# Kernel optimization log

Measured on AMD Instinct MI355X. Metric: run time of the kernel, lower is better.

## Reference

```python
import jax, jax.numpy as jnp
import numpy as np

EPS = 1e-6
ALPHA = 0.2  # LeakyReLU negative slope


def layer_norm(x, g, b):
    mu = jnp.mean(x, axis=-1, keepdims=True)
    var = jnp.mean(jnp.square(x - mu), axis=-1, keepdims=True)
    return (x - mu) * jax.lax.rsqrt(var + EPS) * g + b


def graph_attention(x, bias, W, a_src, a_dst):
    # x: [B,N,D], bias: [B,N,N], W: [D, H*Dh], a_src/a_dst: [H, Dh]
    B, N, D = x.shape
    H, Dh = a_src.shape
    h = jnp.einsum('bnd,dhk->bhnk', x, W.reshape(D, H, Dh))  # [B,H,N,Dh]
    s = jnp.einsum('bhnk,hk->bhn', h, a_src)                 # source term
    t = jnp.einsum('bhnk,hk->bhn', h, a_dst)                 # target term
    e = jax.nn.leaky_relu(s[:, :, :, None] + t[:, :, None, :], ALPHA)
    e = e + bias[:, None, :, :]                              # graph mask/bias
    attn = jax.nn.softmax(e, axis=-1)                        # [B,H,N,N]
    out = jnp.einsum('bhij,bhjk->bhik', attn, h)             # [B,H,N,Dh]
    return out.transpose(0, 2, 1, 3).reshape(B, N, H * Dh)


def setup_inputs() -> dict:
    key = jax.random.key(0)
    ks = jax.random.split(key, 8)
    B, N, D, H = 2, 2048, 512, 8
    Dh = D // H
    sc = 1.0 / np.sqrt(D)
    return {
        'x': jax.random.normal(ks[0], (B, N, D), jnp.float32),
        'bias': jax.random.normal(ks[1], (B, N, N), jnp.float32),
        'W1': jax.random.normal(ks[2], (D, D), jnp.float32) * sc,
        'a_src1': jax.random.normal(ks[3], (H, Dh), jnp.float32) * sc,
        'a_dst1': jax.random.normal(ks[4], (H, Dh), jnp.float32) * sc,
        'g1': jnp.ones((D,), jnp.float32),
        'b1': jnp.zeros((D,), jnp.float32),
        'W2': jax.random.normal(ks[5], (D, D), jnp.float32) * sc,
        'a_src2': jax.random.normal(ks[6], (1, D), jnp.float32) * sc,
        'a_dst2': jax.random.normal(ks[7], (1, D), jnp.float32) * sc,
        'g2': jnp.ones((D,), jnp.float32),
        'b2': jnp.zeros((D,), jnp.float32),
    }


def reference(x, bias, W1, a_src1, a_dst1, g1, b1, W2, a_src2, a_dst2, g2, b2):
    # dropout is identity in eval mode
    attn_in = layer_norm(x, g1, b1)
    attn = graph_attention(attn_in, bias, W1, a_src1, a_dst1) + x
    attn_in2 = layer_norm(attn, g2, b2)
    out = graph_attention(attn_in2, bias, W2, a_src2, a_dst2) + attn
    return out
```

## Files before the change

kernel.cpp:

```cpp
#include <hip/hip_runtime.h>
#include <math.h>

#define NB 2
#define NN 2048
#define DD 512

typedef __attribute__((ext_vector_type(8))) short short8;
typedef __attribute__((ext_vector_type(4))) float f32x4;

__device__ __forceinline__ unsigned short f2bf(float x) {
  union { float f; unsigned u; } a;
  a.f = x;
  unsigned r = a.u + 0x7FFF + ((a.u >> 16) & 1);
  return (unsigned short)(r >> 16);
}
__device__ __forceinline__ float bf2f(unsigned short u) {
  union { unsigned u; float f; } a;
  a.u = ((unsigned)u) << 16;
  return a.f;
}
__device__ __forceinline__ unsigned cvtpk(float lo, float hi) {
  unsigned r;
  asm("v_cvt_pk_bf16_f32 %0, %1, %2" : "=v"(r) : "v"(lo), "v"(hi));
  return r;
}

__device__ __forceinline__ float waveReduceSum(float v) {
#pragma unroll
  for (int o = 32; o; o >>= 1) v += __shfl_down(v, o, 64);
  return v;
}
__device__ __forceinline__ float waveReduceMax(float v) {
#pragma unroll
  for (int o = 32; o; o >>= 1) v = fmaxf(v, __shfl_down(v, o, 64));
  return v;
}
__device__ __forceinline__ float blockReduceSum(float v, float* red4) {
  int tid = threadIdx.x;
  __syncthreads();
  v = waveReduceSum(v);
  if ((tid & 63) == 0) red4[tid >> 6] = v;
  __syncthreads();
  return red4[0] + red4[1] + red4[2] + red4[3];
}
__device__ __forceinline__ float blockReduceMax(float v, float* red4) {
  int tid = threadIdx.x;
  __syncthreads();
  v = waveReduceMax(v);
  if ((tid & 63) == 0) red4[tid >> 6] = v;
  __syncthreads();
  return fmaxf(fmaxf(red4[0], red4[1]), fmaxf(red4[2], red4[3]));
}

__global__ __launch_bounds__(256) void ln_kernel(const float* __restrict__ x,
                                                 const float* __restrict__ g,
                                                 const float* __restrict__ bb,
                                                 unsigned short* __restrict__ y) {
  int row = blockIdx.x;
  int t = threadIdx.x;
  const float* xr = x + (size_t)row * DD;
  __shared__ float red4[4];
  float2 v = *(const float2*)&xr[2 * t];
  float s = blockReduceSum(v.x + v.y, red4);
  float mu = s * (1.0f / 512.0f);
  float d0 = v.x - mu, d1 = v.y - mu;
  float ss = blockReduceSum(d0 * d0 + d1 * d1, red4);
  float rstd = rsqrtf(ss * (1.0f / 512.0f) + 1e-6f);
  float2 gg = *(const float2*)&g[2 * t];
  float2 bv = *(const float2*)&bb[2 * t];
  ushort2 o;
  o.x = f2bf(d0 * rstd * gg.x + bv.x);
  o.y = f2bf(d1 * rstd * gg.y + bv.y);
  *(ushort2*)&y[(size_t)row * DD + 2 * t] = o;
}

__global__ __launch_bounds__(256) void wt2_kernel(const float* __restrict__ W1,
                                                  const float* __restrict__ W2,
                                                  unsigned short* __restrict__ WT1,
                                                  unsigned short* __restrict__ WT2) {
  const float* W = blockIdx.z ? W2 : W1;
  unsigned short* WT = blockIdx.z ? WT2 : WT1;
  __shared__ float tile[64][65];
  int kt = blockIdx.x * 64, ct = blockIdx.y * 64;
  int t = threadIdx.x;
#pragma unroll
  for (int u = 0; u < 16; u++) {
    int lin = t + u * 256;
    int kl = lin >> 6, cl = lin & 63;
    tile[kl][cl] = W[(size_t)(kt + kl) * DD + ct + cl];
  }
  __syncthreads();
#pragma unroll
  for (int u = 0; u < 16; u++) {
    int lin = t + u * 256;
    int cl = lin >> 6, kl = lin & 63;
    WT[(size_t)(ct + cl) * DD + kt + kl] = f2bf(tile[kl][cl]);
  }
}

__global__ __launch_bounds__(256) void v2_kernel(
    const float* __restrict__ W1, const float* __restrict__ as1,
    const float* __restrict__ ad1, float* __restrict__ vs1, float* __restrict__ vd1,
    const float* __restrict__ W2, const float* __restrict__ as2,
    const float* __restrict__ ad2, float* __restrict__ vs2, float* __restrict__ vd2) {
  int slot = blockIdx.y;
  const float *W, *as, *ad;
  float *vs, *vd;
  int Dh, hoff;
  if (slot < 8) {
    W = W1; as = as1 + slot * 64; ad = ad1 + slot * 64;
    vs = vs1 + (size_t)slot * DD; vd = vd1 + (size_t)slot * DD;
    Dh = 64; hoff = slot * 64;
  } else {
    W = W2; as = as2; ad = ad2; vs = vs2; vd = vd2;
    Dh = 512; hoff = 0;
  }
  int t = threadIdx.x;
  int dl = t >> 2, kq = t & 3;
  int d = blockIdx.x * 64 + dl;
  int kn = Dh >> 2;
  const float* wr = W + (size_t)d * DD + hoff + kq * kn;
  const float* asp = as + kq * kn;
  const float* adp = ad + kq * kn;
  float s = 0.f, dd2 = 0.f;
  for (int k = 0; k < kn; k++) {
    float wv = wr[k];
    s += wv * asp[k];
    dd2 += wv * adp[k];
  }
  s += __shfl_xor(s, 1);
  s += __shfl_xor(s, 2);
  dd2 += __shfl_xor(dd2, 1);
  dd2 += __shfl_xor(dd2, 2);
  if (kq == 0) {
    vs[d] = s;
    vd[d] = dd2;
  }
}

__global__ __launch_bounds__(256) void bmax_kernel(const float* __restrict__ bias,
                                                   float* __restrict__ bmax) {
  int row = blockIdx.x;
  int t = threadIdx.x;
  __shared__ float red4[4];
  const float* br = bias + (size_t)row * NN;
  float4 a = *(const float4*)&br[t * 4];
  float4 c = *(const float4*)&br[t * 4 + 1024];
  float lm = fmaxf(fmaxf(fmaxf(a.x, a.y), fmaxf(a.z, a.w)),
                   fmaxf(fmaxf(c.x, c.y), fmaxf(c.z, c.w)));
  float m = blockReduceMax(lm, red4);
  if (t == 0) bmax[row] = m;
}

__global__ __launch_bounds__(256) void gemm_kernel(const unsigned short* __restrict__ A,
                                                   const unsigned short* __restrict__ BT,
                                                   unsigned short* __restrict__ hbT) {
  __shared__ float accL[4][16][65];
  int t = threadIdx.x, w = t >> 6, l = t & 63;
  int li = l & 15, lg = l >> 4;
  int R0 = blockIdx.x * 16;
  int c0 = blockIdx.y * 64;
  const unsigned short* ar = A + (size_t)(R0 + li) * DD + w * 128 + lg * 8;
  const unsigned short* br = BT + (size_t)(c0 + li) * DD + w * 128 + lg * 8;
  f32x4 acc[4] = {};
#pragma unroll
  for (int k0 = 0; k0 < 128; k0 += 32) {
    short8 af = *(const short8*)(ar + k0);
#pragma unroll
    for (int f = 0; f < 4; f++) {
      short8 bf = *(const short8*)(br + (size_t)f * 16 * DD + k0);
      acc[f] = __builtin_amdgcn_mfma_f32_16x16x32_bf16(af, bf, acc[f], 0, 0, 0);
    }
  }
#pragma unroll
  for (int f = 0; f < 4; f++)
#pragma unroll
    for (int r = 0; r < 4; r++) accL[w][lg * 4 + r][f * 16 + li] = acc[f][r];
  __syncthreads();
  int b = R0 >> 11, jT = (R0 & (NN - 1)) >> 4;
  int cT0 = c0 >> 4;
#pragma unroll
  for (int u = 0; u < 2; u++) {
    int idx = t + u * 256;
    int f = idx >> 7;
    int rem = idx & 127;
    int cl = rem >> 3, jlp = rem & 7;
    int cc = f * 16 + cl;
    float v0 = accL[0][2 * jlp][cc] + accL[1][2 * jlp][cc] + accL[2][2 * jlp][cc] +
               accL[3][2 * jlp][cc];
    float v1 = accL[0][2 * jlp + 1][cc] + accL[1][2 * jlp + 1][cc] +
               accL[2][2 * jlp + 1][cc] + accL[3][2 * jlp + 1][cc];
    size_t off = (((size_t)(b * (DD / 16) + cT0 + f) * (NN / 16)) + jT) * 256 +
                 cl * 16 + jlp * 2;
    *(unsigned*)(hbT + off) = cvtpk(v0, v1);
  }
}

__global__ __launch_bounds__(256) void st_kernel(const unsigned short* __restrict__ lnB,
                                                 const float* __restrict__ vs,
                                                 const float* __restrict__ vd,
                                                 float* __restrict__ sOut,
                                                 float* __restrict__ tOut, int HN) {
  int t = threadIdx.x, w = t >> 6, l = t & 63;
  int row = blockIdx.x * 4 + w;
  int b = row >> 11, n = row & (NN - 1);
  const unsigned short* lr = lnB + (size_t)row * DD + l * 8;
  union { short8 v; unsigned short u[8]; } xv;
  xv.v = *(const short8*)lr;
  float xf[8];
#pragma unroll
  for (int k = 0; k < 8; k++) xf[k] = bf2f(xv.u[k]);
  for (int h = 0; h < HN; h++) {
    const float* vsr = vs + (size_t)h * DD + l * 8;
    const float* vdr = vd + (size_t)h * DD + l * 8;
    float4 a0 = *(const float4*)vsr, a1 = *(const float4*)(vsr + 4);
    float4 c0 = *(const float4*)vdr, c1 = *(const float4*)(vdr + 4);
    float ps = xf[0] * a0.x + xf[1] * a0.y + xf[2] * a0.z + xf[3] * a0.w +
               xf[4] * a1.x + xf[5] * a1.y + xf[6] * a1.z + xf[7] * a1.w;
    float pd = xf[0] * c0.x + xf[1] * c0.y + xf[2] * c0.z + xf[3] * c0.w +
               xf[4] * c1.x + xf[5] * c1.y + xf[6] * c1.z + xf[7] * c1.w;
#pragma unroll
    for (int o = 32; o; o >>= 1) {
      ps += __shfl_xor(ps, o);
      pd += __shfl_xor(pd, o);
    }
    if (l == 0) {
      sOut[((size_t)b * HN + h) * NN + n] = ps;
      tOut[((size_t)b * HN + h) * NN + n] = pd;
    }
  }
}

template <int HN>
__global__ __launch_bounds__(256) void pv_kernel(
    const unsigned short* __restrict__ hbT, const float* __restrict__ bias,
    const float* __restrict__ sArr, const float* __restrict__ tArr,
    const float* __restrict__ bmaxA, const float* __restrict__ res,
    float* __restrict__ out) {
  constexpr int DH = DD / HN;
  __shared__ unsigned short Pl[4][1024];
  __shared__ float accL[4][32][33];
  __shared__ float sL[4][32];
  __shared__ float red4[4];
  int t = threadIdx.x, w = t >> 6, l = t & 63;
  int li = l & 15, lg = l >> 4;
  int i0 = blockIdx.x * 32;
  int ck = blockIdx.y, bh = blockIdx.z;
  int h = bh % HN, b = bh / HN;
  int c0 = h * DH + ck * 64;
  size_t bhN = (size_t)bh * NN;
  const float* trow = tArr + bhN;

  float4 ta = *(const float4*)&trow[t * 8];
  float4 tb = *(const float4*)&trow[t * 8 + 4];
  float lm = fmaxf(fmaxf(fmaxf(ta.x, ta.y), fmaxf(ta.z, ta.w)),
                   fmaxf(fmaxf(tb.x, tb.y), fmaxf(tb.z, tb.w)));
  float tmax = blockReduceMax(lm, red4);

  int rs = l >> 3;
  int js = (l & 7) * 4;
  int wq = (((l & 7) >> 1) ^ (rs & 3)) * 8 + (l & 1) * 4;
  float sv[4], Mv[4];
#pragma unroll
  for (int u = 0; u < 4; u++) {
    int row = i0 + u * 8 + rs;
    sv[u] = sArr[bhN + row];
    float q = sv[u] + tmax;
    Mv[u] = fmaxf(q, 0.2f * q) + bmaxA[(size_t)b * NN + row];
  }
  const float* bb = bias + ((size_t)b * NN + i0) * NN;

  const unsigned short* vb =
      hbT + (((size_t)(b * (DD / 16) + (c0 >> 4)) * (NN / 16) + (lg >> 1)) * 256) +
      li * 16 + (lg & 1) * 8;
  int ra0 = li * 32 + ((lg ^ (li & 3)) * 8);
  int ra1 = (16 + li) * 32 + ((lg ^ (li & 3)) * 8);

  const int jbeg = w * (NN / 4), jend = jbeg + NN / 4;
  f32x4 acc[2][4] = {};
  float psum[4] = {0.f, 0.f, 0.f, 0.f};

  float4 ptv = *(const float4*)&trow[jbeg + js];
  float4 pb0 = *(const float4*)&bb[(size_t)(0 * 8 + rs) * NN + jbeg + js];
  float4 pb1 = *(const float4*)&bb[(size_t)(1 * 8 + rs) * NN + jbeg + js];
  float4 pb2 = *(const float4*)&bb[(size_t)(2 * 8 + rs) * NN + jbeg + js];
  float4 pb3 = *(const float4*)&bb[(size_t)(3 * 8 + rs) * NN + jbeg + js];
  short8 nv0 = *(const short8*)(vb + (size_t)jbeg * 16);
  short8 nv1 = *(const short8*)(vb + (size_t)jbeg * 16 + 32768);
  short8 nv2 = *(const short8*)(vb + (size_t)jbeg * 16 + 65536);
  short8 nv3 = *(const short8*)(vb + (size_t)jbeg * 16 + 98304);

  for (int jt = jbeg; jt < jend; jt += 32) {
    float4 tv = ptv;
    float4 bv0 = pb0, bv1 = pb1, bv2 = pb2, bv3 = pb3;
    short8 v0 = nv0, v1 = nv1, v2 = nv2, v3 = nv3;
    if (jt + 32 < jend) {
      int jb = jt + 32 + js;
      ptv = *(const float4*)&trow[jb];
      pb0 = *(const float4*)&bb[(size_t)(0 * 8 + rs) * NN + jb];
      pb1 = *(const float4*)&bb[(size_t)(1 * 8 + rs) * NN + jb];
      pb2 = *(const float4*)&bb[(size_t)(2 * 8 + rs) * NN + jb];
      pb3 = *(const float4*)&bb[(size_t)(3 * 8 + rs) * NN + jb];
      nv0 = *(const short8*)(vb + (size_t)(jt + 32) * 16);
      nv1 = *(const short8*)(vb + (size_t)(jt + 32) * 16 + 32768);
      nv2 = *(const short8*)(vb + (size_t)(jt + 32) * 16 + 65536);
      nv3 = *(const short8*)(vb + (size_t)(jt + 32) * 16 + 98304);
    }
#pragma unroll
    for (int u = 0; u < 4; u++) {
      float4 bv = u == 0 ? bv0 : (u == 1 ? bv1 : (u == 2 ? bv2 : bv3));
      int row = u * 8 + rs;
      float e0 = sv[u] + tv.x;
      float e1 = sv[u] + tv.y;
      float e2 = sv[u] + tv.z;
      float e3 = sv[u] + tv.w;
      e0 = fmaxf(e0, 0.2f * e0) + bv.x;
      e1 = fmaxf(e1, 0.2f * e1) + bv.y;
      e2 = fmaxf(e2, 0.2f * e2) + bv.z;
      e3 = fmaxf(e3, 0.2f * e3) + bv.w;
      float p0 = __expf(e0 - Mv[u]);
      float p1 = __expf(e1 - Mv[u]);
      float p2 = __expf(e2 - Mv[u]);
      float p3 = __expf(e3 - Mv[u]);
      psum[u] += (p0 + p1) + (p2 + p3);
      uint2 d;
      d.x = cvtpk(p0, p1);
      d.y = cvtpk(p2, p3);
      *(uint2*)&Pl[w][row * 32 + wq] = d;
    }
    short8 a0 = *(const short8*)&Pl[w][ra0];
    short8 a1 = *(const short8*)&Pl[w][ra1];
    __builtin_amdgcn_s_setprio(1);
    acc[0][0] = __builtin_amdgcn_mfma_f32_16x16x32_bf16(a0, v0, acc[0][0], 0, 0, 0);
    acc[0][1] = __builtin_amdgcn_mfma_f32_16x16x32_bf16(a0, v1, acc[0][1], 0, 0, 0);
    acc[0][2] = __builtin_amdgcn_mfma_f32_16x16x32_bf16(a0, v2, acc[0][2], 0, 0, 0);
    acc[0][3] = __builtin_amdgcn_mfma_f32_16x16x32_bf16(a0, v3, acc[0][3], 0, 0, 0);
    acc[1][0] = __builtin_amdgcn_mfma_f32_16x16x32_bf16(a1, v0, acc[1][0], 0, 0, 0);
    acc[1][1] = __builtin_amdgcn_mfma_f32_16x16x32_bf16(a1, v1, acc[1][1], 0, 0, 0);
    acc[1][2] = __builtin_amdgcn_mfma_f32_16x16x32_bf16(a1, v2, acc[1][2], 0, 0, 0);
    acc[1][3] = __builtin_amdgcn_mfma_f32_16x16x32_bf16(a1, v3, acc[1][3], 0, 0, 0);
    __builtin_amdgcn_s_setprio(0);
  }
#pragma unroll
  for (int u = 0; u < 4; u++) {
    float r = psum[u];
    r += __shfl_xor(r, 1);
    r += __shfl_xor(r, 2);
    r += __shfl_xor(r, 4);
    if ((l & 7) == 0) sL[w][u * 8 + rs] = r;
  }
#pragma unroll
  for (int rb = 0; rb < 2; rb++)
#pragma unroll
    for (int f = 0; f < 2; f++)
#pragma unroll
      for (int r = 0; r < 4; r++)
        accL[w][rb * 16 + lg * 4 + r][f * 16 + li] = acc[rb][f][r];
  __syncthreads();
  {
    int rr = t >> 3, cc = (t & 7) * 4;
    float S = sL[0][rr] + sL[1][rr] + sL[2][rr] + sL[3][rr];
    float inv = 1.0f / S;
    float4 O;
    O.x = accL[0][rr][cc + 0] + accL[1][rr][cc + 0] + accL[2][rr][cc + 0] + accL[3][rr][cc + 0];
    O.y = accL[0][rr][cc + 1] + accL[1][rr][cc + 1] + accL[2][rr][cc + 1] + accL[3][rr][cc + 1];
    O.z = accL[0][rr][cc + 2] + accL[1][rr][cc + 2] + accL[2][rr][cc + 2] + accL[3][rr][cc + 2];
    O.w = accL[0][rr][cc + 3] + accL[1][rr][cc + 3] + accL[2][rr][cc + 3] + accL[3][rr][cc + 3];
    size_t ix = ((size_t)b * NN + i0 + rr) * DD + c0 + cc;
    float4 rv = *(const float4*)&res[ix];
    float4 ov = {O.x * inv + rv.x, O.y * inv + rv.y, O.z * inv + rv.z, O.w * inv + rv.w};
    *(float4*)&out[ix] = ov;
  }
  __syncthreads();
#pragma unroll
  for (int rb = 0; rb < 2; rb++)
#pragma unroll
    for (int f = 2; f < 4; f++)
#pragma unroll
      for (int r = 0; r < 4; r++)
        accL[w][rb * 16 + lg * 4 + r][(f - 2) * 16 + li] = acc[rb][f][r];
  __syncthreads();
  {
    int rr = t >> 3, cc = (t & 7) * 4;
    float S = sL[0][rr] + sL[1][rr] + sL[2][rr] + sL[3][rr];
    float inv = 1.0f / S;
    float4 O;
    O.x = accL[0][rr][cc + 0] + accL[1][rr][cc + 0] + accL[2][rr][cc + 0] + accL[3][rr][cc + 0];
    O.y = accL[0][rr][cc + 1] + accL[1][rr][cc + 1] + accL[2][rr][cc + 1] + accL[3][rr][cc + 1];
    O.z = accL[0][rr][cc + 2] + accL[1][rr][cc + 2] + accL[2][rr][cc + 2] + accL[3][rr][cc + 2];
    O.w = accL[0][rr][cc + 3] + accL[1][rr][cc + 3] + accL[2][rr][cc + 3] + accL[3][rr][cc + 3];
    size_t ix = ((size_t)b * NN + i0 + rr) * DD + c0 + 32 + cc;
    float4 rv = *(const float4*)&res[ix];
    float4 ov = {O.x * inv + rv.x, O.y * inv + rv.y, O.z * inv + rv.z, O.w * inv + rv.w};
    *(float4*)&out[ix] = ov;
  }
}

extern "C" void kernel_launch(void* const* d_in, const int* in_sizes, int n_in,
                              void* d_out, int out_size, void* d_ws, size_t ws_size,
                              hipStream_t stream) {
  const float* x = (const float*)d_in[0];
  const float* bias = (const float*)d_in[1];
  const float* W1 = (const float*)d_in[2];
  const float* asrc1 = (const float*)d_in[3];
  const float* adst1 = (const float*)d_in[4];
  const float* g1 = (const float*)d_in[5];
  const float* b1 = (const float*)d_in[6];
  const float* W2 = (const float*)d_in[7];
  const float* asrc2 = (const float*)d_in[8];
  const float* adst2 = (const float*)d_in[9];
  const float* g2 = (const float*)d_in[10];
  const float* b2 = (const float*)d_in[11];
  float* out = (float*)d_out;
  float* ws = (float*)d_ws;

  const size_t RC = (size_t)NB * NN * DD;
  float* attnBuf = ws;
  unsigned short* lnB = (unsigned short*)(ws + RC);
  unsigned short* hbT = (unsigned short*)(ws + RC + RC / 2);
  unsigned short* WT1 = (unsigned short*)(ws + 2 * RC);
  unsigned short* WT2 = WT1 + (size_t)DD * DD;
  float* vs1 = (float*)(WT2 + (size_t)DD * DD);
  float* vd1 = vs1 + 8 * DD;
  float* vs2 = vd1 + 8 * DD;
  float* vd2 = vs2 + DD;
  float* sBuf = vd2 + DD;
  float* tBuf = sBuf + 16 * NN;
  float* bmaxB = tBuf + 16 * NN;

  const int rows = NB * NN;

  hipLaunchKernelGGL(wt2_kernel, dim3(8, 8, 2), dim3(256), 0, stream, W1, W2, WT1, WT2);
  hipLaunchKernelGGL(v2_kernel, dim3(8, 9), dim3(256), 0, stream, W1, asrc1, adst1, vs1, vd1,
                     W2, asrc2, adst2, vs2, vd2);
  hipLaunchKernelGGL(bmax_kernel, dim3(rows), dim3(256), 0, stream, bias, bmaxB);

  hipLaunchKernelGGL(ln_kernel, dim3(rows), dim3(256), 0, stream, x, g1, b1, lnB);
  hipLaunchKernelGGL(gemm_kernel, dim3(256, 8), dim3(256), 0, stream, lnB, WT1, hbT);
  hipLaunchKernelGGL(st_kernel, dim3(rows / 4), dim3(256), 0, stream, lnB, vs1, vd1, sBuf, tBuf, 8);
  hipLaunchKernelGGL(pv_kernel<8>, dim3(64, 1, 16), dim3(256), 0, stream, hbT, bias, sBuf,
                     tBuf, bmaxB, x, attnBuf);

  hipLaunchKernelGGL(ln_kernel, dim3(rows), dim3(256), 0, stream, attnBuf, g2, b2, lnB);
  hipLaunchKernelGGL(gemm_kernel, dim3(256, 8), dim3(256), 0, stream, lnB, WT2, hbT);
  hipLaunchKernelGGL(st_kernel, dim3(rows / 4), dim3(256), 0, stream, lnB, vs2, vd2, sBuf, tBuf, 1);
  hipLaunchKernelGGL(pv_kernel<1>, dim3(64, 8, 2), dim3(256), 0, stream, hbT, bias, sBuf,
                     tBuf, bmaxB, attnBuf, out);
}
```

Measured before the change: 160.7 us.

## Store bias as bf16 once and halve pv row tile for more blocks

The bmax pre-pass now also writes a bf16 copy of the bias matrix, and computes the row max from the rounded values so the softmax shift stays consistent. Both pv attention kernels read that bf16 bias, halving bias traffic in the dominant loop. The pv row tile shrinks from 32 to 16 rows with a doubled grid and launch bounds asking for 8 blocks per SM, which raises occupancy but re-reads V twice as often. Rounding the bias to bf16 adds a small numerical error to the attention logits.

```diff
diff --git a/kernel.cpp b/kernel.cpp
--- a/kernel.cpp
+++ b/kernel.cpp
@@ -138,16 +138,28 @@
   }
 }
 
-__global__ __launch_bounds__(256) void bmax_kernel(const float* __restrict__ bias,
-                                                   float* __restrict__ bmax) {
+__global__ __launch_bounds__(256) void bmaxH_kernel(const float* __restrict__ bias,
+                                                    unsigned short* __restrict__ biasH,
+                                                    float* __restrict__ bmax) {
   int row = blockIdx.x;
   int t = threadIdx.x;
   __shared__ float red4[4];
   const float* br = bias + (size_t)row * NN;
   float4 a = *(const float4*)&br[t * 4];
   float4 c = *(const float4*)&br[t * 4 + 1024];
-  float lm = fmaxf(fmaxf(fmaxf(a.x, a.y), fmaxf(a.z, a.w)),
-                   fmaxf(fmaxf(c.x, c.y), fmaxf(c.z, c.w)));
+  uint2 d0, d1;
+  d0.x = cvtpk(a.x, a.y);
+  d0.y = cvtpk(a.z, a.w);
+  d1.x = cvtpk(c.x, c.y);
+  d1.y = cvtpk(c.z, c.w);
+  *(uint2*)&biasH[(size_t)row * NN + t * 4] = d0;
+  *(uint2*)&biasH[(size_t)row * NN + t * 4 + 1024] = d1;
+  union { uint2 v; unsigned short q[4]; } u0, u1;
+  u0.v = d0;
+  u1.v = d1;
+  float lm = -1e30f;
+#pragma unroll
+  for (int k = 0; k < 4; k++) lm = fmaxf(lm, fmaxf(bf2f(u0.q[k]), bf2f(u1.q[k])));
   float m = blockReduceMax(lm, red4);
   if (t == 0) bmax[row] = m;
 }
@@ -232,19 +244,19 @@
 }
 
 template <int HN>
-__global__ __launch_bounds__(256) void pv_kernel(
-    const unsigned short* __restrict__ hbT, const float* __restrict__ bias,
+__global__ __launch_bounds__(256, 8) void pv_kernel(
+    const unsigned short* __restrict__ hbT, const unsigned short* __restrict__ biasH,
     const float* __restrict__ sArr, const float* __restrict__ tArr,
     const float* __restrict__ bmaxA, const float* __restrict__ res,
     float* __restrict__ out) {
   constexpr int DH = DD / HN;
-  __shared__ unsigned short Pl[4][1024];
-  __shared__ float accL[4][32][33];
-  __shared__ float sL[4][32];
+  __shared__ unsigned short Pl[4][512];
+  __shared__ float accL[4][16][33];
+  __shared__ float sL[4][16];
   __shared__ float red4[4];
   int t = threadIdx.x, w = t >> 6, l = t & 63;
   int li = l & 15, lg = l >> 4;
-  int i0 = blockIdx.x * 32;
+  int i0 = blockIdx.x * 16;
   int ck = blockIdx.y, bh = blockIdx.z;
   int h = bh % HN, b = bh / HN;
   int c0 = h * DH + ck * 64;
@@ -260,31 +272,28 @@
   int rs = l >> 3;
   int js = (l & 7) * 4;
   int wq = (((l & 7) >> 1) ^ (rs & 3)) * 8 + (l & 1) * 4;
-  float sv[4], Mv[4];
-#pragma unroll
-  for (int u = 0; u < 4; u++) {
+  float sv[2], Mv[2];
+#pragma unroll
+  for (int u = 0; u < 2; u++) {
     int row = i0 + u * 8 + rs;
     sv[u] = sArr[bhN + row];
     float q = sv[u] + tmax;
     Mv[u] = fmaxf(q, 0.2f * q) + bmaxA[(size_t)b * NN + row];
   }
-  const float* bb = bias + ((size_t)b * NN + i0) * NN;
+  const unsigned short* bbH = biasH + ((size_t)b * NN + i0) * NN;
 
   const unsigned short* vb =
       hbT + (((size_t)(b * (DD / 16) + (c0 >> 4)) * (NN / 16) + (lg >> 1)) * 256) +
       li * 16 + (lg & 1) * 8;
   int ra0 = li * 32 + ((lg ^ (li & 3)) * 8);
-  int ra1 = (16 + li) * 32 + ((lg ^ (li & 3)) * 8);
 
   const int jbeg = w * (NN / 4), jend = jbeg + NN / 4;
-  f32x4 acc[2][4] = {};
-  float psum[4] = {0.f, 0.f, 0.f, 0.f};
+  f32x4 acc[4] = {};
+  float psum[2] = {0.f, 0.f};
 
   float4 ptv = *(const float4*)&trow[jbeg + js];
-  float4 pb0 = *(const float4*)&bb[(size_t)(0 * 8 + rs) * NN + jbeg + js];
-  float4 pb1 = *(const float4*)&bb[(size_t)(1 * 8 + rs) * NN + jbeg + js];
-  float4 pb2 = *(const float4*)&bb[(size_t)(2 * 8 + rs) * NN + jbeg + js];
-  float4 pb3 = *(const float4*)&bb[(size_t)(3 * 8 + rs) * NN + jbeg + js];
+  uint2 pb0 = *(const uint2*)&bbH[(size_t)(0 * 8 + rs) * NN + jbeg + js];
+  uint2 pb1 = *(const uint2*)&bbH[(size_t)(1 * 8 + rs) * NN + jbeg + js];
   short8 nv0 = *(const short8*)(vb + (size_t)jbeg * 16);
   short8 nv1 = *(const short8*)(vb + (size_t)jbeg * 16 + 32768);
   short8 nv2 = *(const short8*)(vb + (size_t)jbeg * 16 + 65536);
@@ -292,32 +301,31 @@
 
   for (int jt = jbeg; jt < jend; jt += 32) {
     float4 tv = ptv;
-    float4 bv0 = pb0, bv1 = pb1, bv2 = pb2, bv3 = pb3;
+    uint2 bq0 = pb0, bq1 = pb1;
     short8 v0 = nv0, v1 = nv1, v2 = nv2, v3 = nv3;
     if (jt + 32 < jend) {
       int jb = jt + 32 + js;
       ptv = *(const float4*)&trow[jb];
-      pb0 = *(const float4*)&bb[(size_t)(0 * 8 + rs) * NN + jb];
-      pb1 = *(const float4*)&bb[(size_t)(1 * 8 + rs) * NN + jb];
-      pb2 = *(const float4*)&bb[(size_t)(2 * 8 + rs) * NN + jb];
-      pb3 = *(const float4*)&bb[(size_t)(3 * 8 + rs) * NN + jb];
+      pb0 = *(const uint2*)&bbH[(size_t)(0 * 8 + rs) * NN + jb];
+      pb1 = *(const uint2*)&bbH[(size_t)(1 * 8 + rs) * NN + jb];
       nv0 = *(const short8*)(vb + (size_t)(jt + 32) * 16);
       nv1 = *(const short8*)(vb + (size_t)(jt + 32) * 16 + 32768);
       nv2 = *(const short8*)(vb + (size_t)(jt + 32) * 16 + 65536);
       nv3 = *(const short8*)(vb + (size_t)(jt + 32) * 16 + 98304);
     }
 #pragma unroll
-    for (int u = 0; u < 4; u++) {
-      float4 bv = u == 0 ? bv0 : (u == 1 ? bv1 : (u == 2 ? bv2 : bv3));
+    for (int u = 0; u < 2; u++) {
+      union { uint2 v; unsigned short q[4]; } bu;
+      bu.v = u ? bq1 : bq0;
       int row = u * 8 + rs;
       float e0 = sv[u] + tv.x;
       float e1 = sv[u] + tv.y;
       float e2 = sv[u] + tv.z;
       float e3 = sv[u] + tv.w;
-      e0 = fmaxf(e0, 0.2f * e0) + bv.x;
-      e1 = fmaxf(e1, 0.2f * e1) + bv.y;
-      e2 = fmaxf(e2, 0.2f * e2) + bv.z;
-      e3 = fmaxf(e3, 0.2f * e3) + bv.w;
+      e0 = fmaxf(e0, 0.2f * e0) + bf2f(bu.q[0]);
+      e1 = fmaxf(e1, 0.2f * e1) + bf2f(bu.q[1]);
+      e2 = fmaxf(e2, 0.2f * e2) + bf2f(bu.q[2]);
+      e3 = fmaxf(e3, 0.2f * e3) + bf2f(bu.q[3]);
       float p0 = __expf(e0 - Mv[u]);
       float p1 = __expf(e1 - Mv[u]);
       float p2 = __expf(e2 - Mv[u]);
@@ -329,20 +337,15 @@
       *(uint2*)&Pl[w][row * 32 + wq] = d;
     }
     short8 a0 = *(const short8*)&Pl[w][ra0];
-    short8 a1 = *(const short8*)&Pl[w][ra1];
     __builtin_amdgcn_s_setprio(1);
-    acc[0][0] = __builtin_amdgcn_mfma_f32_16x16x32_bf16(a0, v0, acc[0][0], 0, 0, 0);
-    acc[0][1] = __builtin_amdgcn_mfma_f32_16x16x32_bf16(a0, v1, acc[0][1], 0, 0, 0);
-    acc[0][2] = __builtin_amdgcn_mfma_f32_16x16x32_bf16(a0, v2, acc[0][2], 0, 0, 0);
-    acc[0][3] = __builtin_amdgcn_mfma_f32_16x16x32_bf16(a0, v3, acc[0][3], 0, 0, 0);
-    acc[1][0] = __builtin_amdgcn_mfma_f32_16x16x32_bf16(a1, v0, acc[1][0], 0, 0, 0);
-    acc[1][1] = __builtin_amdgcn_mfma_f32_16x16x32_bf16(a1, v1, acc[1][1], 0, 0, 0);
-    acc[1][2] = __builtin_amdgcn_mfma_f32_16x16x32_bf16(a1, v2, acc[1][2], 0, 0, 0);
-    acc[1][3] = __builtin_amdgcn_mfma_f32_16x16x32_bf16(a1, v3, acc[1][3], 0, 0, 0);
+    acc[0] = __builtin_amdgcn_mfma_f32_16x16x32_bf16(a0, v0, acc[0], 0, 0, 0);
+    acc[1] = __builtin_amdgcn_mfma_f32_16x16x32_bf16(a0, v1, acc[1], 0, 0, 0);
+    acc[2] = __builtin_amdgcn_mfma_f32_16x16x32_bf16(a0, v2, acc[2], 0, 0, 0);
+    acc[3] = __builtin_amdgcn_mfma_f32_16x16x32_bf16(a0, v3, acc[3], 0, 0, 0);
     __builtin_amdgcn_s_setprio(0);
   }
 #pragma unroll
-  for (int u = 0; u < 4; u++) {
+  for (int u = 0; u < 2; u++) {
     float r = psum[u];
     r += __shfl_xor(r, 1);
     r += __shfl_xor(r, 2);
@@ -350,49 +353,45 @@
     if ((l & 7) == 0) sL[w][u * 8 + rs] = r;
   }
 #pragma unroll
-  for (int rb = 0; rb < 2; rb++)
-#pragma unroll
-    for (int f = 0; f < 2; f++)
-#pragma unroll
-      for (int r = 0; r < 4; r++)
-        accL[w][rb * 16 + lg * 4 + r][f * 16 + li] = acc[rb][f][r];
+  for (int f = 0; f < 2; f++)
+#pragma unroll
+    for (int r = 0; r < 4; r++) accL[w][lg * 4 + r][f * 16 + li] = acc[f][r];
   __syncthreads();
   {
-    int rr = t >> 3, cc = (t & 7) * 4;
+    int rr = t >> 4, cp = (t & 15) * 2;
     float S = sL[0][rr] + sL[1][rr] + sL[2][rr] + sL[3][rr];
     float inv = 1.0f / S;
-    float4 O;
-    O.x = accL[0][rr][cc + 0] + accL[1][rr][cc + 0] + accL[2][rr][cc + 0] + accL[3][rr][cc + 0];
-    O.y = accL[0][rr][cc + 1] + accL[1][rr][cc + 1] + accL[2][rr][cc + 1] + accL[3][rr][cc + 1];
-    O.z = accL[0][rr][cc + 2] + accL[1][rr][cc + 2] + accL[2][rr][cc + 2] + accL[3][rr][cc + 2];
-    O.w = accL[0][rr][cc + 3] + accL[1][rr][cc + 3] + accL[2][rr][cc + 3] + accL[3][rr][cc + 3];
-    size_t ix = ((size_t)b * NN + i0 + rr) * DD + c0 + cc;
-    float4 rv = *(const float4*)&res[ix];
-    float4 ov = {O.x * inv + rv.x, O.y * inv + rv.y, O.z * inv + rv.z, O.w * inv + rv.w};
-    *(float4*)&out[ix] = ov;
-  }
-  __syncthreads();
-#pragma unroll
-  for (int rb = 0; rb < 2; rb++)
-#pragma unroll
-    for (int f = 2; f < 4; f++)
-#pragma unroll
-      for (int r = 0; r < 4; r++)
-        accL[w][rb * 16 + lg * 4 + r][(f - 2) * 16 + li] = acc[rb][f][r];
+    float2 O = {0.f, 0.f};
+#pragma unroll
+    for (int w2 = 0; w2 < 4; w2++) {
+      O.x += accL[w2][rr][cp];
+      O.y += accL[w2][rr][cp + 1];
+    }
+    size_t ix = ((size_t)b * NN + i0 + rr) * DD + c0 + cp;
+    float2 rv = *(const float2*)&res[ix];
+    float2 ov = {O.x * inv + rv.x, O.y * inv + rv.y};
+    *(float2*)&out[ix] = ov;
+  }
+  __syncthreads();
+#pragma unroll
+  for (int f = 2; f < 4; f++)
+#pragma unroll
+    for (int r = 0; r < 4; r++) accL[w][lg * 4 + r][(f - 2) * 16 + li] = acc[f][r];
   __syncthreads();
   {
-    int rr = t >> 3, cc = (t & 7) * 4;
+    int rr = t >> 4, cp = (t & 15) * 2;
     float S = sL[0][rr] + sL[1][rr] + sL[2][rr] + sL[3][rr];
     float inv = 1.0f / S;
-    float4 O;
-    O.x = accL[0][rr][cc + 0] + accL[1][rr][cc + 0] + accL[2][rr][cc + 0] + accL[3][rr][cc + 0];
-    O.y = accL[0][rr][cc + 1] + accL[1][rr][cc + 1] + accL[2][rr][cc + 1] + accL[3][rr][cc + 1];
-    O.z = accL[0][rr][cc + 2] + accL[1][rr][cc + 2] + accL[2][rr][cc + 2] + accL[3][rr][cc + 2];
-    O.w = accL[0][rr][cc + 3] + accL[1][rr][cc + 3] + accL[2][rr][cc + 3] + accL[3][rr][cc + 3];
-    size_t ix = ((size_t)b * NN + i0 + rr) * DD + c0 + 32 + cc;
-    float4 rv = *(const float4*)&res[ix];
-    float4 ov = {O.x * inv + rv.x, O.y * inv + rv.y, O.z * inv + rv.z, O.w * inv + rv.w};
-    *(float4*)&out[ix] = ov;
+    float2 O = {0.f, 0.f};
+#pragma unroll
+    for (int w2 = 0; w2 < 4; w2++) {
+      O.x += accL[w2][rr][cp];
+      O.y += accL[w2][rr][cp + 1];
+    }
+    size_t ix = ((size_t)b * NN + i0 + rr) * DD + c0 + 32 + cp;
+    float2 rv = *(const float2*)&res[ix];
+    float2 ov = {O.x * inv + rv.x, O.y * inv + rv.y};
+    *(float2*)&out[ix] = ov;
   }
 }
 
@@ -427,23 +426,24 @@
   float* sBuf = vd2 + DD;
   float* tBuf = sBuf + 16 * NN;
   float* bmaxB = tBuf + 16 * NN;
+  unsigned short* biasH = (unsigned short*)(bmaxB + (size_t)NB * NN);
 
   const int rows = NB * NN;
 
   hipLaunchKernelGGL(wt2_kernel, dim3(8, 8, 2), dim3(256), 0, stream, W1, W2, WT1, WT2);
   hipLaunchKernelGGL(v2_kernel, dim3(8, 9), dim3(256), 0, stream, W1, asrc1, adst1, vs1, vd1,
                      W2, asrc2, adst2, vs2, vd2);
-  hipLaunchKernelGGL(bmax_kernel, dim3(rows), dim3(256), 0, stream, bias, bmaxB);
+  hipLaunchKernelGGL(bmaxH_kernel, dim3(rows), dim3(256), 0, stream, bias, biasH, bmaxB);
 
   hipLaunchKernelGGL(ln_kernel, dim3(rows), dim3(256), 0, stream, x, g1, b1, lnB);
   hipLaunchKernelGGL(gemm_kernel, dim3(256, 8), dim3(256), 0, stream, lnB, WT1, hbT);
   hipLaunchKernelGGL(st_kernel, dim3(rows / 4), dim3(256), 0, stream, lnB, vs1, vd1, sBuf, tBuf, 8);
-  hipLaunchKernelGGL(pv_kernel<8>, dim3(64, 1, 16), dim3(256), 0, stream, hbT, bias, sBuf,
+  hipLaunchKernelGGL(pv_kernel<8>, dim3(128, 1, 16), dim3(256), 0, stream, hbT, biasH, sBuf,
                      tBuf, bmaxB, x, attnBuf);
 
   hipLaunchKernelGGL(ln_kernel, dim3(rows), dim3(256), 0, stream, attnBuf, g2, b2, lnB);
   hipLaunchKernelGGL(gemm_kernel, dim3(256, 8), dim3(256), 0, stream, lnB, WT2, hbT);
   hipLaunchKernelGGL(st_kernel, dim3(rows / 4), dim3(256), 0, stream, lnB, vs2, vd2, sBuf, tBuf, 1);
-  hipLaunchKernelGGL(pv_kernel<1>, dim3(64, 8, 2), dim3(256), 0, stream, hbT, bias, sBuf,
+  hipLaunchKernelGGL(pv_kernel<1>, dim3(128, 8, 2), dim3(256), 0, stream, hbT, biasH, sBuf,
                      tBuf, bmaxB, attnBuf, out);
 }
```

Result: slower. 601.1 us (+274.1%).
